# Performance work log

Hardware: AMD Instinct MI355X
Metric: run time of the kernel (lower is better)

## Reference

```python
import jax, jax.numpy as jnp
import numpy as np

B, NQ, NUM_CLASSES, K = 64, 300, 80, 150
NC = 4 + NUM_CLASSES  # channels per query
POOL = 32             # 640 -> 20 spatial via 32x32 mean pooling (surrogate backbone)


def setup_inputs() -> dict:
    key = jax.random.key(0)
    k1, k2 = jax.random.split(key)
    x = jax.random.randint(k1, (B, 3, 640, 640), 0, 256, dtype=jnp.int32)  # uint8-like image
    W = jax.random.normal(k2, (3 * 20 * 20, NQ * NC), dtype=jnp.float32) * 0.02
    return {"x": x, "W": W}


def reference(x, W):
    # --- preprocessing (faithful to original) ---
    xf = x.astype(jnp.float32) / 255.0
    xf = xf[:, jnp.array([2, 1, 0]), :, :]  # BGR -> RGB

    # --- opaque backbone surrogate: avg-pool 640->20, flatten, linear ---
    b, c, h, w = xf.shape
    pooled = xf.reshape(b, c, h // POOL, POOL, w // POOL, POOL).mean(axis=(3, 5))  # [B,3,20,20]
    y = (pooled.reshape(b, -1) @ W).reshape(-1, NQ, NC)  # [B,300,84]

    # --- postprocessing chain (the kernel target) ---
    boxes = y[:, :, :4]           # [B,300,4]
    class_scores = y[:, :, 4:]    # [B,300,80]
    max_scores = class_scores.max(axis=2)      # [B,300]
    class_ids = class_scores.argmax(axis=2)    # [B,300] (first-index ties, same as torch.max)
    topk_scores, topk_idx = jax.lax.top_k(max_scores, K)  # sorted descending, as torch.topk(sorted=True)
    topk_boxes = jnp.take_along_axis(boxes, topk_idx[:, :, None], axis=1)  # [B,K,4]
    topk_ids = jnp.take_along_axis(class_ids, topk_idx, axis=1)            # [B,K]
    return jnp.concatenate(
        [topk_boxes, topk_scores[:, :, None], topk_ids[:, :, None].astype(jnp.float32)],
        axis=2,
    )  # [B,K,6]
```

## Files before the change

### kernel.cpp

```cpp
#include <hip/hip_runtime.h>
#include <stdint.h>

#define BATCH 64
#define NQ 300
#define NCH 84
#define KTOP 150
#define NTOT (NQ * NCH)
#define KDIM 1200
#define NCHUNK 4
#define KCH 300
#define HW 640
#define PF 6

#define WS_Y   614400
#define WS_SC  52224000
#define WS_CID 52377600

__global__ __launch_bounds__(256) void pool_kernel(const int* __restrict__ x,
                                                   double* __restrict__ At) {
  int wave = threadIdx.x >> 6;
  int lane = threadIdx.x & 63;
  int cell = blockIdx.x * 4 + wave;
  int b   = cell / 1200;
  int rem = cell - b * 1200;
  int cin = rem / 400;
  int pp  = rem - cin * 400;
  int ph = pp / 20, pw = pp - ph * 20;
  const int* base = x + (((b * 3 + cin) * HW) + ph * 32) * HW + pw * 32;
  int r  = lane >> 1;
  int c0 = (lane & 1) * 16;
  const int4* p = (const int4*)(base + r * HW + c0);
  int4 v0 = p[0], v1 = p[1], v2 = p[2], v3 = p[3];
  int s = v0.x + v0.y + v0.z + v0.w + v1.x + v1.y + v1.z + v1.w
        + v2.x + v2.y + v2.z + v2.w + v3.x + v3.y + v3.z + v3.w;
  #pragma unroll
  for (int off = 32; off > 0; off >>= 1) s += __shfl_down(s, off);
  if (lane == 0) {
    int kout = (2 - cin) * 400 + pp;
    At[kout * 64 + b] = (double)s * (1.0 / 261120.0);
  }
}

__global__ __launch_bounds__(512) void gemm_kernel(const double* __restrict__ At,
                                                   const float* __restrict__ W,
                                                   double* __restrict__ Y) {
  int wave  = threadIdx.x >> 6;
  int lane  = threadIdx.x & 63;
  int chunk = blockIdx.y;
  int row0  = __builtin_amdgcn_readfirstlane((int)(wave * 8));
  int n  = blockIdx.x * 128 + 2 * lane;
  int nl = n < NTOT - 1 ? n : NTOT - 2;
  const double2* Ap = (const double2*)(At + (size_t)chunk * KCH * 64 + row0);
  const float*   Wp = W + (size_t)chunk * KCH * NTOT + nl;
  double acc0[8], acc1[8];
  #pragma unroll
  for (int i = 0; i < 8; ++i) { acc0[i] = 0.0; acc1[i] = 0.0; }
  float2 w[PF];
  #pragma unroll
  for (int u = 0; u < PF; ++u) w[u] = *(const float2*)(Wp + (size_t)u * NTOT);
  #pragma unroll 1
  for (int k0 = 0; k0 < KCH; k0 += PF) {
    int kn = (k0 + PF == KCH) ? 0 : k0 + PF;
    float2 wn[PF];
    #pragma unroll
    for (int u = 0; u < PF; ++u) wn[u] = *(const float2*)(Wp + (size_t)(kn + u) * NTOT);
    #pragma unroll
    for (int u = 0; u < PF; ++u) {
      double wd0 = (double)w[u].x;
      double wd1 = (double)w[u].y;
      #pragma unroll
      for (int j = 0; j < 4; ++j) {
        double2 a = Ap[(size_t)(k0 + u) * 32 + j];
        acc0[2 * j]     = fma(a.x, wd0, acc0[2 * j]);
        acc1[2 * j]     = fma(a.x, wd1, acc1[2 * j]);
        acc0[2 * j + 1] = fma(a.y, wd0, acc0[2 * j + 1]);
        acc1[2 * j + 1] = fma(a.y, wd1, acc1[2 * j + 1]);
      }
    }
    #pragma unroll
    for (int u = 0; u < PF; ++u) w[u] = wn[u];
  }
  if (n < NTOT) {
    double* Yp = Y + ((size_t)chunk * BATCH + row0) * NTOT + n;
    #pragma unroll
    for (int i = 0; i < 8; ++i) {
      double2 o; o.x = acc0[i]; o.y = acc1[i];
      *(double2*)(Yp + (size_t)i * NTOT) = o;
    }
  }
}

__global__ __launch_bounds__(256) void argmax_kernel(const double* __restrict__ Y,
                                                     double* __restrict__ sc,
                                                     int* __restrict__ cid) {
  int wave = threadIdx.x >> 6;
  int lane = threadIdx.x & 63;
  int task = blockIdx.x * 4 + wave;
  int b = task / NQ;
  int q = task - b * NQ;
  const double* y = Y + (size_t)b * NTOT + q * NCH;
  const size_t P = (size_t)BATCH * NTOT;
  double best = ((y[4 + lane] + y[P + 4 + lane]) + y[2 * P + 4 + lane]) + y[3 * P + 4 + lane];
  int    cls  = lane;
  if (lane < 16) {
    double v2 = ((y[68 + lane] + y[P + 68 + lane]) + y[2 * P + 68 + lane]) + y[3 * P + 68 + lane];
    if (v2 > best) { best = v2; cls = 64 + lane; }
  }
  #pragma unroll
  for (int off = 32; off > 0; off >>= 1) {
    double ob = __shfl_down(best, off);
    int    oc = __shfl_down(cls, off);
    if (ob > best || (ob == best && oc < cls)) { best = ob; cls = oc; }
  }
  if (lane == 0) { sc[task] = best; cid[task] = cls; }
}

__global__ __launch_bounds__(256) void select_kernel(const double* __restrict__ Y,
                                                     const double* __restrict__ sc,
                                                     const int* __restrict__ cid,
                                                     float* __restrict__ out) {
  __shared__ double ssc[NQ];
  __shared__ int    scid[NQ];
  int b = blockIdx.x;
  int t = threadIdx.x;
  for (int q = t; q < NQ; q += 256) {
    ssc[q]  = sc[b * NQ + q];
    scid[q] = cid[b * NQ + q];
  }
  __syncthreads();
  const size_t P = (size_t)BATCH * NTOT;
  for (int q = t; q < NQ; q += 256) {
    double s = ssc[q];
    int rank = 0;
    for (int j = 0; j < NQ; ++j) {
      double sj = ssc[j];
      rank += (sj > s) || (sj == s && j < q);
    }
    if (rank < KTOP) {
      const double* r0 = Y + (size_t)b * NTOT + q * NCH;
      float* o = out + ((size_t)b * KTOP + rank) * 6;
      o[0] = (float)(((r0[0] + r0[P + 0]) + r0[2 * P + 0]) + r0[3 * P + 0]);
      o[1] = (float)(((r0[1] + r0[P + 1]) + r0[2 * P + 1]) + r0[3 * P + 1]);
      o[2] = (float)(((r0[2] + r0[P + 2]) + r0[2 * P + 2]) + r0[3 * P + 2]);
      o[3] = (float)(((r0[3] + r0[P + 3]) + r0[2 * P + 3]) + r0[3 * P + 3]);
      o[4] = (float)s;
      o[5] = (float)scid[q];
    }
  }
}

extern "C" void kernel_launch(void* const* d_in, const int* in_sizes, int n_in,
                              void* d_out, int out_size, void* d_ws, size_t ws_size,
                              hipStream_t stream) {
  const int*   x = (const int*)d_in[0];
  const float* W = (const float*)d_in[1];
  double* At  = (double*)d_ws;
  double* Y   = (double*)((char*)d_ws + WS_Y);
  double* sc  = (double*)((char*)d_ws + WS_SC);
  int*    cid = (int*)((char*)d_ws + WS_CID);
  pool_kernel<<<dim3(19200), dim3(256), 0, stream>>>(x, At);
  gemm_kernel<<<dim3(197, NCHUNK), dim3(512), 0, stream>>>(At, W, Y);
  argmax_kernel<<<dim3(4800), dim3(256), 0, stream>>>(Y, sc, cid);
  select_kernel<<<dim3(64), dim3(256), 0, stream>>>(Y, sc, cid, (float*)d_out);
}
```

Baseline: 592.7 us.

## Switch GEMM to fp32 with fp64 rescue for near-tie scores

The fp64 GEMM and its intermediate buffer become fp32, which halves Y traffic and uses faster fp32 FMA. Two new kernels keep the ranking close to the fp64 result. One flags queries whose argmax margin or score gap to another query falls below set thresholds. The other recomputes those flagged scores in fp64 straight from W. This adds two launches and a per-batch O(NQ^2) scan, and correctness now depends on fixed error thresholds.

```diff
diff --git a/kernel.cpp b/kernel.cpp
--- a/kernel.cpp
+++ b/kernel.cpp
@@ -12,12 +12,20 @@
 #define HW 640
 #define PF 6
 
-#define WS_Y   614400
-#define WS_SC  52224000
-#define WS_CID 52377600
+#define MARGIN_ARGMAX 1e-4f
+#define PAIR_BASE     2e-5f
+#define PAIR_INFLATE  1.2e-4f
+
+#define WS_AF   614400
+#define WS_YF   921600
+#define WS_SC   26726400
+#define WS_SC32 26880000
+#define WS_CID  26956800
+#define WS_FLG  27033600
 
 __global__ __launch_bounds__(256) void pool_kernel(const int* __restrict__ x,
-                                                   double* __restrict__ At) {
+                                                   double* __restrict__ At,
+                                                   float* __restrict__ Af) {
   int wave = threadIdx.x >> 6;
   int lane = threadIdx.x & 63;
   int cell = blockIdx.x * 4 + wave;
@@ -38,23 +46,24 @@
   if (lane == 0) {
     int kout = (2 - cin) * 400 + pp;
     At[kout * 64 + b] = (double)s * (1.0 / 261120.0);
-  }
-}
-
-__global__ __launch_bounds__(512) void gemm_kernel(const double* __restrict__ At,
+    Af[kout * 64 + b] = (float)s * (1.0f / 261120.0f);
+  }
+}
+
+__global__ __launch_bounds__(512) void gemm_kernel(const float* __restrict__ Af,
                                                    const float* __restrict__ W,
-                                                   double* __restrict__ Y) {
+                                                   float* __restrict__ Yf) {
   int wave  = threadIdx.x >> 6;
   int lane  = threadIdx.x & 63;
   int chunk = blockIdx.y;
   int row0  = __builtin_amdgcn_readfirstlane((int)(wave * 8));
   int n  = blockIdx.x * 128 + 2 * lane;
   int nl = n < NTOT - 1 ? n : NTOT - 2;
-  const double2* Ap = (const double2*)(At + (size_t)chunk * KCH * 64 + row0);
-  const float*   Wp = W + (size_t)chunk * KCH * NTOT + nl;
-  double acc0[8], acc1[8];
-  #pragma unroll
-  for (int i = 0; i < 8; ++i) { acc0[i] = 0.0; acc1[i] = 0.0; }
+  const float4* Ap = (const float4*)(Af + (size_t)chunk * KCH * 64 + row0);
+  const float*  Wp = W + (size_t)chunk * KCH * NTOT + nl;
+  float acc0[8], acc1[8];
+  #pragma unroll
+  for (int i = 0; i < 8; ++i) { acc0[i] = 0.0f; acc1[i] = 0.0f; }
   float2 w[PF];
   #pragma unroll
   for (int u = 0; u < PF; ++u) w[u] = *(const float2*)(Wp + (size_t)u * NTOT);
@@ -66,56 +75,139 @@
     for (int u = 0; u < PF; ++u) wn[u] = *(const float2*)(Wp + (size_t)(kn + u) * NTOT);
     #pragma unroll
     for (int u = 0; u < PF; ++u) {
-      double wd0 = (double)w[u].x;
-      double wd1 = (double)w[u].y;
-      #pragma unroll
-      for (int j = 0; j < 4; ++j) {
-        double2 a = Ap[(size_t)(k0 + u) * 32 + j];
-        acc0[2 * j]     = fma(a.x, wd0, acc0[2 * j]);
-        acc1[2 * j]     = fma(a.x, wd1, acc1[2 * j]);
-        acc0[2 * j + 1] = fma(a.y, wd0, acc0[2 * j + 1]);
-        acc1[2 * j + 1] = fma(a.y, wd1, acc1[2 * j + 1]);
-      }
+      float w0 = w[u].x, w1 = w[u].y;
+      float4 a0 = Ap[(k0 + u) * 16 + 0];
+      float4 a1 = Ap[(k0 + u) * 16 + 1];
+      acc0[0] = fmaf(a0.x, w0, acc0[0]);  acc1[0] = fmaf(a0.x, w1, acc1[0]);
+      acc0[1] = fmaf(a0.y, w0, acc0[1]);  acc1[1] = fmaf(a0.y, w1, acc1[1]);
+      acc0[2] = fmaf(a0.z, w0, acc0[2]);  acc1[2] = fmaf(a0.z, w1, acc1[2]);
+      acc0[3] = fmaf(a0.w, w0, acc0[3]);  acc1[3] = fmaf(a0.w, w1, acc1[3]);
+      acc0[4] = fmaf(a1.x, w0, acc0[4]);  acc1[4] = fmaf(a1.x, w1, acc1[4]);
+      acc0[5] = fmaf(a1.y, w0, acc0[5]);  acc1[5] = fmaf(a1.y, w1, acc1[5]);
+      acc0[6] = fmaf(a1.z, w0, acc0[6]);  acc1[6] = fmaf(a1.z, w1, acc1[6]);
+      acc0[7] = fmaf(a1.w, w0, acc0[7]);  acc1[7] = fmaf(a1.w, w1, acc1[7]);
     }
     #pragma unroll
     for (int u = 0; u < PF; ++u) w[u] = wn[u];
   }
   if (n < NTOT) {
-    double* Yp = Y + ((size_t)chunk * BATCH + row0) * NTOT + n;
+    float* Yp = Yf + ((size_t)chunk * BATCH + row0) * NTOT + n;
     #pragma unroll
     for (int i = 0; i < 8; ++i) {
-      double2 o; o.x = acc0[i]; o.y = acc1[i];
-      *(double2*)(Yp + (size_t)i * NTOT) = o;
-    }
-  }
-}
-
-__global__ __launch_bounds__(256) void argmax_kernel(const double* __restrict__ Y,
+      float2 o; o.x = acc0[i]; o.y = acc1[i];
+      *(float2*)(Yp + (size_t)i * NTOT) = o;
+    }
+  }
+}
+
+__global__ __launch_bounds__(256) void argmax_kernel(const float* __restrict__ Yf,
+                                                     double* __restrict__ sc,
+                                                     float* __restrict__ sc32,
+                                                     int* __restrict__ cid,
+                                                     int* __restrict__ flg) {
+  int wave = threadIdx.x >> 6;
+  int lane = threadIdx.x & 63;
+  int task = blockIdx.x * 4 + wave;
+  int b = task / NQ;
+  int q = task - b * NQ;
+  const float* y = Yf + (size_t)b * NTOT + q * NCH;
+  const size_t P = (size_t)BATCH * NTOT;
+  float v1 = ((y[4 + lane] + y[P + 4 + lane]) + y[2 * P + 4 + lane]) + y[3 * P + 4 + lane];
+  float best = v1;
+  float sec  = -1e30f;
+  int   cls  = lane;
+  if (lane < 16) {
+    float v2 = ((y[68 + lane] + y[P + 68 + lane]) + y[2 * P + 68 + lane]) + y[3 * P + 68 + lane];
+    if (v2 > best) { sec = best; best = v2; cls = 64 + lane; }
+    else           { sec = v2; }
+  }
+  #pragma unroll
+  for (int off = 32; off > 0; off >>= 1) {
+    float ob = __shfl_down(best, off);
+    float os = __shfl_down(sec, off);
+    int   oc = __shfl_down(cls, off);
+    if (ob > best || (ob == best && oc < cls)) {
+      sec = fmaxf(best, os); best = ob; cls = oc;
+    } else {
+      sec = fmaxf(ob, sec);
+    }
+  }
+  if (lane == 0) {
+    sc[task]   = (double)best;
+    sc32[task] = best;
+    cid[task]  = cls;
+    flg[task]  = (best - sec < MARGIN_ARGMAX) ? 1 : 0;
+  }
+}
+
+__global__ __launch_bounds__(256) void pairscan_kernel(const float* __restrict__ sc32,
+                                                       int* __restrict__ flg) {
+  __shared__ float s[NQ];
+  __shared__ int   f[NQ];
+  int b = blockIdx.x;
+  int t = threadIdx.x;
+  for (int q = t; q < NQ; q += 256) {
+    s[q] = sc32[b * NQ + q];
+    f[q] = flg[b * NQ + q];
+  }
+  __syncthreads();
+  for (int q = t; q < NQ; q += 256) {
+    float sq = s[q];
+    int   fq = f[q];
+    int   hit = 0;
+    for (int j = 0; j < NQ; ++j) {
+      float thr = PAIR_BASE + (((fq | f[j]) & 1) ? PAIR_INFLATE : 0.0f);
+      hit |= (j != q) & (fabsf(sq - s[j]) < thr);
+    }
+    if (hit) flg[b * NQ + q] = fq | 2;
+  }
+}
+
+__global__ __launch_bounds__(256) void rescue_kernel(const double* __restrict__ At,
+                                                     const float* __restrict__ W,
+                                                     const int* __restrict__ flg,
                                                      double* __restrict__ sc,
                                                      int* __restrict__ cid) {
   int wave = threadIdx.x >> 6;
   int lane = threadIdx.x & 63;
   int task = blockIdx.x * 4 + wave;
+  int f = flg[task];
+  if (f == 0) return;
   int b = task / NQ;
   int q = task - b * NQ;
-  const double* y = Y + (size_t)b * NTOT + q * NCH;
-  const size_t P = (size_t)BATCH * NTOT;
-  double best = ((y[4 + lane] + y[P + 4 + lane]) + y[2 * P + 4 + lane]) + y[3 * P + 4 + lane];
-  int    cls  = lane;
-  if (lane < 16) {
-    double v2 = ((y[68 + lane] + y[P + 68 + lane]) + y[2 * P + 68 + lane]) + y[3 * P + 68 + lane];
-    if (v2 > best) { best = v2; cls = 64 + lane; }
-  }
-  #pragma unroll
-  for (int off = 32; off > 0; off >>= 1) {
-    double ob = __shfl_down(best, off);
-    int    oc = __shfl_down(cls, off);
-    if (ob > best || (ob == best && oc < cls)) { best = ob; cls = oc; }
-  }
-  if (lane == 0) { sc[task] = best; cid[task] = cls; }
-}
-
-__global__ __launch_bounds__(256) void select_kernel(const double* __restrict__ Y,
+  if (f & 1) {
+    const float* Wq = W + q * NCH + 4;
+    double a1 = 0.0, a2 = 0.0;
+    for (int k = 0; k < KDIM; ++k) {
+      double a = At[k * 64 + b];
+      a1 = fma(a, (double)Wq[(size_t)k * NTOT + lane], a1);
+      if (lane < 16)
+        a2 = fma(a, (double)Wq[(size_t)k * NTOT + 64 + lane], a2);
+    }
+    double best = a1;
+    int    cls  = lane;
+    if (lane < 16 && a2 > best) { best = a2; cls = 64 + lane; }
+    #pragma unroll
+    for (int off = 32; off > 0; off >>= 1) {
+      double ob = __shfl_down(best, off);
+      int    oc = __shfl_down(cls, off);
+      if (ob > best || (ob == best && oc < cls)) { best = ob; cls = oc; }
+    }
+    if (lane == 0) { sc[task] = best; cid[task] = cls; }
+  } else {
+    const float* Wc = W + q * NCH + 4 + cid[task];
+    double s = 0.0;
+    for (int t = 0; t < 19; ++t) {
+      int k = lane + 64 * t;
+      if (k < KDIM) s = fma(At[k * 64 + b], (double)Wc[(size_t)k * NTOT], s);
+    }
+    #pragma unroll
+    for (int off = 32; off > 0; off >>= 1) s += __shfl_xor(s, off);
+    if (lane == 0) sc[task] = s;
+  }
+}
+
+__global__ __launch_bounds__(256) void select_kernel(const float* __restrict__ Yf,
                                                      const double* __restrict__ sc,
                                                      const int* __restrict__ cid,
                                                      float* __restrict__ out) {
@@ -137,12 +229,12 @@
       rank += (sj > s) || (sj == s && j < q);
     }
     if (rank < KTOP) {
-      const double* r0 = Y + (size_t)b * NTOT + q * NCH;
+      const float* r0 = Yf + (size_t)b * NTOT + q * NCH;
       float* o = out + ((size_t)b * KTOP + rank) * 6;
-      o[0] = (float)(((r0[0] + r0[P + 0]) + r0[2 * P + 0]) + r0[3 * P + 0]);
-      o[1] = (float)(((r0[1] + r0[P + 1]) + r0[2 * P + 1]) + r0[3 * P + 1]);
-      o[2] = (float)(((r0[2] + r0[P + 2]) + r0[2 * P + 2]) + r0[3 * P + 2]);
-      o[3] = (float)(((r0[3] + r0[P + 3]) + r0[2 * P + 3]) + r0[3 * P + 3]);
+      o[0] = ((r0[0] + r0[P + 0]) + r0[2 * P + 0]) + r0[3 * P + 0];
+      o[1] = ((r0[1] + r0[P + 1]) + r0[2 * P + 1]) + r0[3 * P + 1];
+      o[2] = ((r0[2] + r0[P + 2]) + r0[2 * P + 2]) + r0[3 * P + 2];
+      o[3] = ((r0[3] + r0[P + 3]) + r0[2 * P + 3]) + r0[3 * P + 3];
       o[4] = (float)s;
       o[5] = (float)scid[q];
     }
@@ -154,12 +246,17 @@
                               hipStream_t stream) {
   const int*   x = (const int*)d_in[0];
   const float* W = (const float*)d_in[1];
-  double* At  = (double*)d_ws;
-  double* Y   = (double*)((char*)d_ws + WS_Y);
-  double* sc  = (double*)((char*)d_ws + WS_SC);
-  int*    cid = (int*)((char*)d_ws + WS_CID);
-  pool_kernel<<<dim3(19200), dim3(256), 0, stream>>>(x, At);
-  gemm_kernel<<<dim3(197, NCHUNK), dim3(512), 0, stream>>>(At, W, Y);
-  argmax_kernel<<<dim3(4800), dim3(256), 0, stream>>>(Y, sc, cid);
-  select_kernel<<<dim3(64), dim3(256), 0, stream>>>(Y, sc, cid, (float*)d_out);
-}
+  double* At   = (double*)d_ws;
+  float*  Af   = (float*)((char*)d_ws + WS_AF);
+  float*  Yf   = (float*)((char*)d_ws + WS_YF);
+  double* sc   = (double*)((char*)d_ws + WS_SC);
+  float*  sc32 = (float*)((char*)d_ws + WS_SC32);
+  int*    cid  = (int*)((char*)d_ws + WS_CID);
+  int*    flg  = (int*)((char*)d_ws + WS_FLG);
+  pool_kernel<<<dim3(19200), dim3(256), 0, stream>>>(x, At, Af);
+  gemm_kernel<<<dim3(197, NCHUNK), dim3(512), 0, stream>>>(Af, W, Yf);
+  argmax_kernel<<<dim3(4800), dim3(256), 0, stream>>>(Yf, sc, sc32, cid, flg);
+  pairscan_kernel<<<dim3(64), dim3(256), 0, stream>>>(sc32, flg);
+  rescue_kernel<<<dim3(4800), dim3(256), 0, stream>>>(At, W, flg, sc, cid);
+  select_kernel<<<dim3(64), dim3(256), 0, stream>>>(Yf, sc, cid, (float*)d_out);
+}
```

New measurement: 927.2 us. +56.4%, slower.
